# Performance work log

Hardware: AMD Instinct MI355X
Metric: run time of the kernel (lower is better)

## Reference

```python
import jax, jax.numpy as jnp
import numpy as np

DIM = 180
HEADS = 6
HID = 360
WINDOWS = ((8, 8), (16, 16))
SHIFTS0 = ((0, 0), (0, 0))
SHIFTS1 = ((4, 4), (8, 8))
EPS = 1e-5


def _bn(x, g, b, m, v):
    # eval-mode BatchNorm2d over [B,C,H,W]
    inv = g / jnp.sqrt(v + EPS)
    return x * inv[None, :, None, None] + (b - m * inv)[None, :, None, None]


def _conv1x1(x, w, b):
    return jnp.einsum('oc,bchw->bohw', w, x) + b[None, :, None, None]


def _shift_plus(x):
    # ShiftConv2d1x1 masked depthwise 3x3 == zero-padded single-pixel shifts per channel block
    c = x.shape[1] // 5
    pad = lambda a, spec: jnp.pad(a, ((0, 0), (0, 0)) + spec)
    g0 = pad(x[:, 0 * c:1 * c, :, 1:], ((0, 0), (0, 1)))   # out[y,x] = in[y,x+1]
    g1 = pad(x[:, 1 * c:2 * c, :, :-1], ((0, 0), (1, 0)))  # in[y,x-1]
    g2 = pad(x[:, 2 * c:3 * c, 1:, :], ((0, 1), (0, 0)))   # in[y+1,x]
    g3 = pad(x[:, 3 * c:4 * c, :-1, :], ((1, 0), (0, 0)))  # in[y-1,x]
    g4 = x[:, 4 * c:]
    return jnp.concatenate([g0, g1, g2, g3, g4], axis=1)


def _mlp(x, w1, b1, w2, b2):
    h = _conv1x1(_shift_plus(x), w1, b1)
    h = jax.nn.gelu(h, approximate=False)
    return _conv1x1(_shift_plus(h), w2, b2)


def _pixel_mixer(x):
    # circular-pad masked depthwise conv == circular rolls, channels interleaved mod 5
    B, C, H, W = x.shape
    xr = x.reshape(B, C // 5, 5, H, W)
    g0 = jnp.roll(xr[:, :, 0], -1, axis=-1)  # mask[m,2m]: in[y,(x+1)%W]
    g1 = jnp.roll(xr[:, :, 1], 1, axis=-1)   # mask[m,0]:  in[y,(x-1)%W]
    g2 = jnp.roll(xr[:, :, 2], -1, axis=-2)  # mask[2m,m]: in[(y+1)%H,x]
    g3 = jnp.roll(xr[:, :, 3], 1, axis=-2)   # mask[0,m]:  in[(y-1)%H,x]
    g4 = xr[:, :, 4]
    return jnp.stack([g0, g1, g2, g3, g4], axis=2).reshape(B, C, H, W)


def _swsa_slice(s, ws, shift):
    B, C, h, w = s.shape
    ph, pw = (-h) % ws[0], (-w) % ws[1]
    if ph or pw:
        s = jnp.pad(s, ((0, 0), (0, 0), (0, ph), (0, pw)), mode='reflect')
    if shift != (0, 0):
        s = jnp.roll(s, shift, axis=(2, 3))
    H, W = s.shape[2], s.shape[3]
    nh, nw = H // ws[0], W // ws[1]
    c = C // (2 * HEADS)
    # b (qv head c) (nh ws1) (nw ws2) -> qv b head nh nw (ws1 ws2) c
    s = s.reshape(B, 2, HEADS, c, nh, ws[0], nw, ws[1])
    s = s.transpose(1, 0, 2, 4, 6, 5, 7, 3).reshape(2, B, HEADS, nh, nw, ws[0] * ws[1], c)
    q, v = s[0], s[1]
    attn = jax.nn.softmax(jnp.einsum('...ic,...jc->...ij', q, q), axis=-1)
    o = jnp.einsum('...ij,...jc->...ic', attn, v)
    # -> b (head c) (nh ws1) (nw ws2)
    o = o.reshape(B, HEADS, nh, nw, ws[0], ws[1], c)
    o = o.transpose(0, 1, 6, 2, 4, 3, 5).reshape(B, HEADS * c, H, W)
    if shift != (0, 0):
        o = jnp.roll(o, (-shift[0], -shift[1]), axis=(2, 3))
    return o[:, :, :h, :w]


def _swsa(x, qkv_w, qkv_b, bn_g, bn_b, bn_m, bn_v, proj_w, proj_b, shifts):
    qkv = _bn(_conv1x1(x, qkv_w, qkv_b), bn_g, bn_b, bn_m, bn_v)
    C = qkv.shape[1]
    n = len(WINDOWS)
    outs = [_swsa_slice(qkv[:, i * (C // n):(i + 1) * (C // n)], ws, sh)
            for i, (ws, sh) in enumerate(zip(WINDOWS, shifts))]
    return _conv1x1(jnp.concatenate(outs, axis=1), proj_w, proj_b)


def _forward(x, a0_qkv_w, a0_qkv_b, a0_bn_g, a0_bn_b, a0_bn_m, a0_bn_v, a0_proj_w, a0_proj_b,
             a1_qkv_w, a1_qkv_b, a1_bn_g, a1_bn_b, a1_bn_m, a1_bn_v, a1_proj_w, a1_proj_b,
             t2_bn_g, t2_bn_b, t2_bn_m, t2_bn_v,
             m0_fc1_w, m0_fc1_b, m0_fc2_w, m0_fc2_b,
             m1_fc1_w, m1_fc1_b, m1_fc2_w, m1_fc2_b,
             m2_fc1_w, m2_fc1_b, m2_fc2_w, m2_fc2_b):
    # layer 0: SWSA (no shift) + Mlp
    x = x + _swsa(x, a0_qkv_w, a0_qkv_b, a0_bn_g, a0_bn_b, a0_bn_m, a0_bn_v, a0_proj_w, a0_proj_b, SHIFTS0)
    x = x + _mlp(x, m0_fc1_w, m0_fc1_b, m0_fc2_w, m0_fc2_b)
    # layer 1: SWSA (shifted) + Mlp
    x = x + _swsa(x, a1_qkv_w, a1_qkv_b, a1_bn_g, a1_bn_b, a1_bn_m, a1_bn_v, a1_proj_w, a1_proj_b, SHIFTS1)
    x = x + _mlp(x, m1_fc1_w, m1_fc1_b, m1_fc2_w, m1_fc2_b)
    # layer 2: TokenMixer + Mlp
    x = x + _bn(_pixel_mixer(x) - x, t2_bn_g, t2_bn_b, t2_bn_m, t2_bn_v)
    x = x + _mlp(x, m2_fc1_w, m2_fc1_b, m2_fc2_w, m2_fc2_b)
    return x


def setup_inputs() -> dict:
    keys = iter(jax.random.split(jax.random.key(0), 64))
    nrm = lambda s: jax.random.normal(next(keys), s, jnp.float32) * 0.02
    d, hd = DIM, HID
    inp = {'x': jax.random.normal(next(keys), (1, d, 256, 256), jnp.float32)}
    for i in range(2):
        inp[f'a{i}_qkv_w'] = nrm((2 * d, d))
        inp[f'a{i}_qkv_b'] = jnp.zeros((2 * d,), jnp.float32)
        inp[f'a{i}_bn_g'] = jnp.ones((2 * d,), jnp.float32)
        inp[f'a{i}_bn_b'] = jnp.zeros((2 * d,), jnp.float32)
        inp[f'a{i}_bn_m'] = jnp.zeros((2 * d,), jnp.float32)
        inp[f'a{i}_bn_v'] = jnp.ones((2 * d,), jnp.float32)
        inp[f'a{i}_proj_w'] = nrm((d, d))
        inp[f'a{i}_proj_b'] = jnp.zeros((d,), jnp.float32)
    inp['t2_bn_g'] = jnp.ones((d,), jnp.float32)
    inp['t2_bn_b'] = jnp.zeros((d,), jnp.float32)
    inp['t2_bn_m'] = jnp.zeros((d,), jnp.float32)
    inp['t2_bn_v'] = jnp.ones((d,), jnp.float32)
    for i in range(3):
        inp[f'm{i}_fc1_w'] = nrm((hd, d))
        inp[f'm{i}_fc1_b'] = jnp.zeros((hd,), jnp.float32)
        inp[f'm{i}_fc2_w'] = nrm((d, hd))
        inp[f'm{i}_fc2_b'] = jnp.zeros((d,), jnp.float32)
    return inp


def reference(x, a0_qkv_w, a0_qkv_b, a0_bn_g, a0_bn_b, a0_bn_m, a0_bn_v, a0_proj_w, a0_proj_b,
              a1_qkv_w, a1_qkv_b, a1_bn_g, a1_bn_b, a1_bn_m, a1_bn_v, a1_proj_w, a1_proj_b,
              t2_bn_g, t2_bn_b, t2_bn_m, t2_bn_v,
              m0_fc1_w, m0_fc1_b, m0_fc2_w, m0_fc2_b,
              m1_fc1_w, m1_fc1_b, m1_fc2_w, m1_fc2_b,
              m2_fc1_w, m2_fc1_b, m2_fc2_w, m2_fc2_b):
    return _forward(x, a0_qkv_w, a0_qkv_b, a0_bn_g, a0_bn_b, a0_bn_m, a0_bn_v, a0_proj_w, a0_proj_b,
                    a1_qkv_w, a1_qkv_b, a1_bn_g, a1_bn_b, a1_bn_m, a1_bn_v, a1_proj_w, a1_proj_b,
                    t2_bn_g, t2_bn_b, t2_bn_m, t2_bn_v,
                    m0_fc1_w, m0_fc1_b, m0_fc2_w, m0_fc2_b,
                    m1_fc1_w, m1_fc1_b, m1_fc2_w, m1_fc2_b,
                    m2_fc1_w, m2_fc1_b, m2_fc2_w, m2_fc2_b)
```

## Files before the change

kernel.cpp:

```cpp
#include <hip/hip_runtime.h>
#include <hip/hip_bf16.h>
#include <math.h>

#define P 65536

typedef float f32x4 __attribute__((ext_vector_type(4)));
typedef float f32x16 __attribute__((ext_vector_type(16)));
typedef short bf16x8 __attribute__((ext_vector_type(8)));
typedef unsigned short us8 __attribute__((ext_vector_type(8)));

__device__ __forceinline__ unsigned short f2b(float f) {
    __hip_bfloat16 h = __float2bfloat16(f);
    return __builtin_bit_cast(unsigned short, h);
}
__device__ __forceinline__ float b2f(unsigned short h) {
    return __builtin_bit_cast(float, (unsigned)h << 16);
}
__device__ __forceinline__ int shift_src(int g, int p) {
    int h = p >> 8, w = p & 255;
    if (g == 0) return (w < 255) ? p + 1 : -1;
    if (g == 1) return (w > 0) ? p - 1 : -1;
    if (g == 2) return (h < 255) ? p + 256 : -1;
    if (g == 3) return (h > 0) ? p - 256 : -1;
    return p;
}
__device__ __forceinline__ ushort4 cvt4(float4 f) {
    ushort4 o = {f2b(f.x), f2b(f.y), f2b(f.z), f2b(f.w)};
    return o;
}

__global__ __launch_bounds__(256) void to_nhwc(const float* __restrict__ x,
                                               unsigned short* __restrict__ Xb) {
    const int p = blockIdx.x * 256 + threadIdx.x;
    const int by = blockIdx.y;
    #pragma unroll
    for (int i = 0; i < 9; i++) {
        const int c4 = by * 9 + i;
        float4 v;
        v.x = x[(size_t)(c4 * 4 + 0) * P + p];
        v.y = x[(size_t)(c4 * 4 + 1) * P + p];
        v.z = x[(size_t)(c4 * 4 + 2) * P + p];
        v.w = x[(size_t)(c4 * 4 + 3) * P + p];
        *(ushort4*)&Xb[(size_t)p * 192 + c4 * 4] = cvt4(v);
    }
    if (by == 4) {
        ushort4 z4 = {0, 0, 0, 0};
        *(ushort4*)&Xb[(size_t)p * 192 + 180] = z4;
        *(ushort4*)&Xb[(size_t)p * 192 + 184] = z4;
        *(ushort4*)&Xb[(size_t)p * 192 + 188] = z4;
    }
}

struct WJobs {
    const float* W[10];
    const float* Bi[10];
    const float* G[10];
    const float* Bb[10];
    const float* M[10];
    const float* V[10];
    unsigned short* Wb[10];
    float* Sc[10];
    float* Sh[10];
    int OC[10];
    int K[10];
};
__global__ __launch_bounds__(256) void wcvtAll(WJobs j) {
    const int m = blockIdx.y;
    const int K = j.K[m];
    const int KP = (K == 180) ? 192 : 384;
    const int idx = blockIdx.x * 256 + threadIdx.x;
    if (idx >= 384 * KP) return;
    const int r = idx / KP, kp = idx - r * KP;
    const int rl = r % 192, rp = r / 192;
    const int kl = kp % 192, kpl = kp / 192;
    const int oc = (rl < 180) ? rp * 180 + rl : -1;
    const int k  = (kl < 180) ? kpl * 180 + kl : -1;
    const bool vld = (oc >= 0 && oc < j.OC[m]);
    unsigned short v = 0;
    if (vld && k >= 0 && k < K) v = f2b(j.W[m][(size_t)oc * K + k]);
    j.Wb[m][idx] = v;
    if (kp == 0) {
        float sc = 1.f, sh = 0.f;
        if (vld) {
            if (j.G[m]) {
                float inv = j.G[m][oc] * rsqrtf(j.V[m][oc] + 1e-5f);
                sc = inv;
                sh = j.Bb[m][oc] + (j.Bi[m][oc] - j.M[m][oc]) * inv;
            } else {
                sh = j.Bi[m][oc];
            }
        }
        j.Sc[m][r] = sc;
        j.Sh[m][r] = sh;
    }
}

template<int CIN, int SHIFT, int GELU, int RES, int CHW>
__global__ __launch_bounds__(512, 4) void mconv(
    const unsigned short* __restrict__ X0, const unsigned short* __restrict__ X1,
    const unsigned short* __restrict__ Wb,
    const float* __restrict__ Sc, const float* __restrict__ Sh,
    const unsigned short* __restrict__ Res,
    unsigned short* __restrict__ OutB0, unsigned short* __restrict__ OutB1,
    float* __restrict__ OutF)
{
    constexpr int KP = (CIN == 180) ? 192 : 384;
    constexpr int NCH = KP / 64;

    __shared__ __align__(16) unsigned short lx[128][76];
    __shared__ __align__(16) unsigned short lw[192][76];

    const int tid = threadIdx.x;
    const int lane = tid & 63, wid = tid >> 6;
    const int wp = wid >> 2, wo = wid & 3;
    const int pbase = blockIdx.x * 128;
    const int pl = blockIdx.y;
    Wb += (size_t)pl * 192 * KP;
    Sc += pl * 192;
    Sh += pl * 192;
    unsigned short* __restrict__ OutB = pl ? OutB1 : OutB0;

    f32x4 acc[3][4];
    #pragma unroll
    for (int a = 0; a < 3; a++)
        #pragma unroll
        for (int b = 0; b < 4; b++) acc[a][b] = (f32x4){0.f, 0.f, 0.f, 0.f};

    for (int ch = 0; ch < NCH; ++ch) {
        const int kc0 = ch * 64;
        if (ch) __syncthreads();
        #pragma unroll
        for (int i = 0; i < 3; i++) {
            int idx = tid + i * 512;
            int row = idx >> 3, c8 = (idx & 7) * 8;
            *(us8*)&lw[row][c8] = *(const us8*)&Wb[(size_t)row * KP + kc0 + c8];
        }
        if constexpr (CIN == 180 && !SHIFT) {
            #pragma unroll
            for (int i = 0; i < 2; i++) {
                int idx = tid + i * 512;
                int row = idx >> 3, c8 = (idx & 7) * 8;
                *(us8*)&lx[row][c8] = *(const us8*)&X0[(size_t)(pbase + row) * 192 + kc0 + c8];
            }
        } else if constexpr (CIN == 180) {
            #pragma unroll
            for (int i = 0; i < 4; i++) {
                int idx = tid + i * 512;
                int row = idx >> 4, c4 = kc0 + (idx & 15) * 4;
                int p = pbase + row;
                ushort4 hv = {0, 0, 0, 0};
                if (c4 < 180) {
                    int sp = shift_src(c4 / 36, p);
                    if (sp >= 0) hv = *(const ushort4*)&X0[(size_t)sp * 192 + c4];
                }
                *(ushort4*)&lx[row][c4 - kc0] = hv;
            }
        } else {
            const bool pl1 = (kc0 >= 192);
            const unsigned short* __restrict__ Xp = pl1 ? X1 : X0;
            const int kbase = kc0 - (pl1 ? 192 : 0);
            #pragma unroll
            for (int i = 0; i < 4; i++) {
                int idx = tid + i * 512;
                int row = idx >> 4, c4l = kbase + (idx & 15) * 4;
                int p = pbase + row;
                ushort4 hv = {0, 0, 0, 0};
                int k = (pl1 ? 180 : 0) + c4l;
                if (c4l < 180) {
                    if constexpr (SHIFT) {
                        int sp = shift_src(k / 72, p);
                        if (sp >= 0) hv = *(const ushort4*)&Xp[(size_t)sp * 192 + c4l];
                    } else {
                        hv = *(const ushort4*)&Xp[(size_t)p * 192 + c4l];
                    }
                }
                *(ushort4*)&lx[row][c4l - kbase] = hv;
            }
        }
        __syncthreads();
        #pragma unroll
        for (int ks = 0; ks < 2; ++ks) {
            const int ko = ks * 32 + (lane >> 4) * 8;
            bf16x8 av[3], bvv[4];
            #pragma unroll
            for (int m = 0; m < 3; m++)
                av[m] = *(const bf16x8*)&lw[wo * 48 + m * 16 + (lane & 15)][ko];
            #pragma unroll
            for (int n = 0; n < 4; n++)
                bvv[n] = *(const bf16x8*)&lx[wp * 64 + n * 16 + (lane & 15)][ko];
            #pragma unroll
            for (int m = 0; m < 3; m++)
                #pragma unroll
                for (int n = 0; n < 4; n++)
                    acc[m][n] = __builtin_amdgcn_mfma_f32_16x16x32_bf16(
                        av[m], bvv[n], acc[m][n], 0, 0, 0);
        }
    }

    #pragma unroll
    for (int m = 0; m < 3; ++m) {
        const int oc0 = wo * 48 + m * 16 + ((lane >> 4) * 4);
        if (oc0 >= 180) continue;
        float4 sc4 = *(const float4*)&Sc[oc0];
        float4 sh4 = *(const float4*)&Sh[oc0];
        #pragma unroll
        for (int n = 0; n < 4; ++n) {
            const int pix = pbase + wp * 64 + n * 16 + (lane & 15);
            float4 y;
            y.x = acc[m][n][0] * sc4.x + sh4.x;
            y.y = acc[m][n][1] * sc4.y + sh4.y;
            y.z = acc[m][n][2] * sc4.z + sh4.z;
            y.w = acc[m][n][3] * sc4.w + sh4.w;
            if constexpr (GELU) {
                y.x = 0.5f * y.x * (1.f + erff(y.x * 0.70710678118654752f));
                y.y = 0.5f * y.y * (1.f + erff(y.y * 0.70710678118654752f));
                y.z = 0.5f * y.z * (1.f + erff(y.z * 0.70710678118654752f));
                y.w = 0.5f * y.w * (1.f + erff(y.w * 0.70710678118654752f));
            }
            if constexpr (RES) {
                ushort4 rv = *(const ushort4*)&Res[(size_t)pix * 192 + oc0];
                y.x += b2f(rv.x);
                y.y += b2f(rv.y);
                y.z += b2f(rv.z);
                y.w += b2f(rv.w);
            }
            if constexpr (CHW) {
                OutF[(size_t)(oc0 + 0) * P + pix] = y.x;
                OutF[(size_t)(oc0 + 1) * P + pix] = y.y;
                OutF[(size_t)(oc0 + 2) * P + pix] = y.z;
                OutF[(size_t)(oc0 + 3) * P + pix] = y.w;
            } else {
                *(ushort4*)&OutB[(size_t)pix * 192 + oc0] = cvt4(y);
            }
        }
    }
}

template<int WSZ>
__device__ __forceinline__ void attn_body(const unsigned short* __restrict__ Qp,
                                          unsigned short* __restrict__ Ov, int sh,
                                          int bx, unsigned short* smem)
{
    constexpr int TOK = WSZ * WSZ;
    constexpr int WPB = (WSZ == 8) ? 4 : 1;
    constexpr int NMI = TOK / 32;

    unsigned short (*q_s)[24] = (unsigned short(*)[24])smem;
    unsigned short (*v_s)[16] = (unsigned short(*)[16])(smem + WPB * TOK * 24);

    const int tid = threadIdx.x;
    const int lane = tid & 63, wid = tid >> 6;
    const int la = lane & 31, h = lane >> 5;
    const int head = blockIdx.y;
    const int qoff = head * 15;
    const int obase = ((WSZ == 8) ? 0 : 90) + head * 15;

    const int win = (WSZ == 8) ? (bx * 4 + wid) : bx;
    const int wy = win >> ((WSZ == 8) ? 5 : 4);
    const int wx = win & ((WSZ == 8) ? 31 : 15);

    {
        const int sw = (WSZ == 8) ? wid : 0;
        const int t = (WSZ == 8) ? (tid & 63) : tid;
        const int ty = t / WSZ, tx = t % WSZ;
        const int gh = (wy * WSZ + ty - sh) & 255;
        const int gw = (wx * WSZ + tx - sh) & 255;
        const unsigned short* src = Qp + (size_t)((gh << 8) | gw) * 192 + qoff;
        #pragma unroll
        for (int c = 0; c < 15; c++) {
            q_s[sw * TOK + t][c] = src[c];
            v_s[sw * TOK + t][c] = src[90 + c];
        }
        q_s[sw * TOK + t][15] = 0;
        v_s[sw * TOK + t][15] = 0;
    }
    __syncthreads();

    const int mywin = (WSZ == 8) ? wid : 0;
    const unsigned short (*qs)[24] = &q_s[mywin * TOK];
    const unsigned short (*vs)[16] = &v_s[mywin * TOK];
    const int ni0 = (WSZ == 8) ? 0 : (wid * 2);
    const int ni1 = ni0 + 1;

    bf16x8 bfr0 = *(const bf16x8*)&qs[ni0 * 32 + la][h * 8];
    bf16x8 bfr1 = *(const bf16x8*)&qs[ni1 * 32 + la][h * 8];

    f32x16 O0, O1;
    #pragma unroll
    for (int r = 0; r < 16; r++) { O0[r] = 0.f; O1[r] = 0.f; }
    float m0 = -3.0e38f, m1 = -3.0e38f, l0 = 0.f, l1 = 0.f;

    unsigned short hw0[16], hw1[16];

    auto proc = [&](f32x16& S, float& m, float& l, f32x16& O, unsigned short* hw) {
        float vm = S[0];
        #pragma unroll
        for (int r = 1; r < 16; r++) vm = fmaxf(vm, S[r]);
        vm = fmaxf(vm, __shfl_xor(vm, 32));
        float nm = fmaxf(m, vm);
        float rs = __expf(m - nm);
        m = nm;
        l *= rs;
        #pragma unroll
        for (int r = 0; r < 16; r++) O[r] *= rs;
        float lacc = 0.f;
        #pragma unroll
        for (int r = 0; r < 16; r++) {
            unsigned short u = f2b(__expf(S[r] - nm));
            hw[r] = u;
            lacc += b2f(u);
        }
        l += lacc;
    };

    auto pack = [&](const unsigned short* hw, int sub) -> bf16x8 {
        unsigned A01 = (unsigned)hw[8 * sub + 0] | ((unsigned)hw[8 * sub + 1] << 16);
        unsigned A23 = (unsigned)hw[8 * sub + 2] | ((unsigned)hw[8 * sub + 3] << 16);
        unsigned B01 = (unsigned)hw[8 * sub + 4] | ((unsigned)hw[8 * sub + 5] << 16);
        unsigned B23 = (unsigned)hw[8 * sub + 6] | ((unsigned)hw[8 * sub + 7] << 16);
        unsigned x1 = (unsigned)__shfl_xor((int)(h ? A01 : B01), 32);
        unsigned x2 = (unsigned)__shfl_xor((int)(h ? A23 : B23), 32);
        union { unsigned u[4]; bf16x8 v; } pf;
        pf.u[0] = h ? x1 : A01;
        pf.u[1] = h ? x2 : A23;
        pf.u[2] = h ? B01 : x1;
        pf.u[3] = h ? B23 : x2;
        return pf.v;
    };

    for (int mi = 0; mi < NMI; ++mi) {
        bf16x8 af = *(const bf16x8*)&qs[mi * 32 + la][h * 8];
        f32x16 z;
        #pragma unroll
        for (int r = 0; r < 16; r++) z[r] = 0.f;
        f32x16 s0 = __builtin_amdgcn_mfma_f32_32x32x16_bf16(af, bfr0, z, 0, 0, 0);
        f32x16 s1 = __builtin_amdgcn_mfma_f32_32x32x16_bf16(af, bfr1, z, 0, 0, 0);

        proc(s0, m0, l0, O0, hw0);
        proc(s1, m1, l1, O1, hw1);

        #pragma unroll
        for (int sub = 0; sub < 2; ++sub) {
            union { unsigned short us[8]; bf16x8 v; } av;
            #pragma unroll
            for (int j = 0; j < 8; j++)
                av.us[j] = vs[mi * 32 + sub * 16 + h * 8 + j][la & 15];
            bf16x8 pf0 = pack(hw0, sub);
            bf16x8 pf1 = pack(hw1, sub);
            O0 = __builtin_amdgcn_mfma_f32_32x32x16_bf16(av.v, pf0, O0, 0, 0, 0);
            O1 = __builtin_amdgcn_mfma_f32_32x32x16_bf16(av.v, pf1, O1, 0, 0, 0);
        }
    }

    #pragma unroll
    for (int t = 0; t < 2; ++t) {
        const f32x16& O = t ? O1 : O0;
        float l = t ? l1 : l0;
        const int ni = t ? ni1 : ni0;
        float lt = l + __shfl_xor(l, 32);
        float inv = 1.f / lt;
        const int R = ni * 32 + la;
        const int ty = R / WSZ, tx = R % WSZ;
        const int gh = (wy * WSZ + ty - sh) & 255;
        const int gw = (wx * WSZ + tx - sh) & 255;
        unsigned short* dst = Ov + (size_t)((gh << 8) | gw) * 192 + obase;
        #pragma unroll
        for (int reg = 0; reg < 16; ++reg) {
            const int ch = (reg & 3) + 8 * (reg >> 2) + 4 * h;
            if (ch < 15) dst[ch] = f2b(O[reg] * inv);
        }
    }
}

__global__ __launch_bounds__(256) void mattn2(const unsigned short* __restrict__ Q0,
                                              const unsigned short* __restrict__ Q1,
                                              unsigned short* __restrict__ Av,
                                              int sh8, int sh16)
{
    __shared__ __align__(16) unsigned short smem[10240];
    if (blockIdx.x < 256) attn_body<8>(Q0, Av, sh8, blockIdx.x, smem);
    else                  attn_body<16>(Q1, Av, sh16, blockIdx.x - 256, smem);
}

__global__ __launch_bounds__(256) void pixmixk(const unsigned short* __restrict__ Xb,
    const float* __restrict__ g, const float* __restrict__ b,
    const float* __restrict__ m, const float* __restrict__ v,
    unsigned short* __restrict__ Yb)
{
    const int idx = blockIdx.x * 256 + threadIdx.x;
    const int p = idx / 45;
    const int c0 = (idx - p * 45) * 4;
    const int h = p >> 8, w = p & 255;
    ushort4 xv4 = *(const ushort4*)&Xb[(size_t)p * 192 + c0];
    ushort4 o;
    #pragma unroll
    for (int j = 0; j < 4; j++) {
        int c = c0 + j;
        int gr = c - (c / 5) * 5;
        int sp;
        if (gr == 0)      sp = (h << 8) | ((w + 1) & 255);
        else if (gr == 1) sp = (h << 8) | ((w - 1) & 255);
        else if (gr == 2) sp = (((h + 1) & 255) << 8) | w;
        else if (gr == 3) sp = (((h - 1) & 255) << 8) | w;
        else              sp = p;
        float pm = b2f(Xb[(size_t)sp * 192 + c]);
        float xv = b2f(((const unsigned short*)&xv4)[j]);
        float inv = g[c] * rsqrtf(v[c] + 1e-5f);
        float y = xv + (pm - xv - m[c]) * inv + b[c];
        ((unsigned short*)&o)[j] = f2b(y);
    }
    *(ushort4*)&Yb[(size_t)p * 192 + c0] = o;
}

extern "C" void kernel_launch(void* const* d_in, const int* in_sizes, int n_in,
                              void* d_out, int out_size, void* d_ws, size_t ws_size,
                              hipStream_t stream)
{
    const float* x        = (const float*)d_in[0];
    const float* a0_qkv_w = (const float*)d_in[1];
    const float* a0_qkv_b = (const float*)d_in[2];
    const float* a0_bn_g  = (const float*)d_in[3];
    const float* a0_bn_b  = (const float*)d_in[4];
    const float* a0_bn_m  = (const float*)d_in[5];
    const float* a0_bn_v  = (const float*)d_in[6];
    const float* a0_proj_w= (const float*)d_in[7];
    const float* a0_proj_b= (const float*)d_in[8];
    const float* a1_qkv_w = (const float*)d_in[9];
    const float* a1_qkv_b = (const float*)d_in[10];
    const float* a1_bn_g  = (const float*)d_in[11];
    const float* a1_bn_b  = (const float*)d_in[12];
    const float* a1_bn_m  = (const float*)d_in[13];
    const float* a1_bn_v  = (const float*)d_in[14];
    const float* a1_proj_w= (const float*)d_in[15];
    const float* a1_proj_b= (const float*)d_in[16];
    const float* t2_bn_g  = (const float*)d_in[17];
    const float* t2_bn_b  = (const float*)d_in[18];
    const float* t2_bn_m  = (const float*)d_in[19];
    const float* t2_bn_v  = (const float*)d_in[20];
    const float* m0_fc1_w = (const float*)d_in[21];
    const float* m0_fc1_b = (const float*)d_in[22];
    const float* m0_fc2_w = (const float*)d_in[23];
    const float* m0_fc2_b = (const float*)d_in[24];
    const float* m1_fc1_w = (const float*)d_in[25];
    const float* m1_fc1_b = (const float*)d_in[26];
    const float* m1_fc2_w = (const float*)d_in[27];
    const float* m1_fc2_b = (const float*)d_in[28];
    const float* m2_fc1_w = (const float*)d_in[29];
    const float* m2_fc1_b = (const float*)d_in[30];
    const float* m2_fc2_w = (const float*)d_in[31];
    const float* m2_fc2_b = (const float*)d_in[32];

    unsigned short* Q0  = (unsigned short*)d_ws;
    unsigned short* Q1  = Q0 + (size_t)P * 192;
    unsigned short* Ob  = Q1 + (size_t)P * 192;
    unsigned short* Av  = Ob + (size_t)P * 192;
    unsigned short* Wp  = Av + (size_t)P * 192;
    const size_t W192 = 384 * 192, W384 = (size_t)384 * 384;
    unsigned short* wb_qkv0 = Wp;
    unsigned short* wb_prj0 = wb_qkv0 + W192;
    unsigned short* wb_qkv1 = wb_prj0 + W192;
    unsigned short* wb_prj1 = wb_qkv1 + W192;
    unsigned short* wb_fc1_0 = wb_prj1 + W192;
    unsigned short* wb_fc1_1 = wb_fc1_0 + W192;
    unsigned short* wb_fc1_2 = wb_fc1_1 + W192;
    unsigned short* wb_fc2_0 = wb_fc1_2 + W192;
    unsigned short* wb_fc2_1 = wb_fc2_0 + W384;
    unsigned short* wb_fc2_2 = wb_fc2_1 + W384;
    float* ScA = (float*)(wb_fc2_2 + W384);
    float* ShA = ScA + 10 * 384;

    dim3 blk(256);
    dim3 blk512(512);
    dim3 gA(512, 2);
    dim3 gB(512);
    dim3 gAt(512, 6);

    WJobs jobs;
    for (int i = 0; i < 10; i++) { jobs.G[i] = nullptr; jobs.Bb[i] = nullptr; jobs.M[i] = nullptr; jobs.V[i] = nullptr; }
    jobs.W[0] = a0_qkv_w;  jobs.Bi[0] = a0_qkv_b;  jobs.Wb[0] = wb_qkv0;  jobs.OC[0] = 360; jobs.K[0] = 180;
    jobs.G[0] = a0_bn_g; jobs.Bb[0] = a0_bn_b; jobs.M[0] = a0_bn_m; jobs.V[0] = a0_bn_v;
    jobs.W[1] = a0_proj_w; jobs.Bi[1] = a0_proj_b; jobs.Wb[1] = wb_prj0;  jobs.OC[1] = 180; jobs.K[1] = 180;
    jobs.W[2] = a1_qkv_w;  jobs.Bi[2] = a1_qkv_b;  jobs.Wb[2] = wb_qkv1;  jobs.OC[2] = 360; jobs.K[2] = 180;
    jobs.G[2] = a1_bn_g; jobs.Bb[2] = a1_bn_b; jobs.M[2] = a1_bn_m; jobs.V[2] = a1_bn_v;
    jobs.W[3] = a1_proj_w; jobs.Bi[3] = a1_proj_b; jobs.Wb[3] = wb_prj1;  jobs.OC[3] = 180; jobs.K[3] = 180;
    jobs.W[4] = m0_fc1_w;  jobs.Bi[4] = m0_fc1_b;  jobs.Wb[4] = wb_fc1_0; jobs.OC[4] = 360; jobs.K[4] = 180;
    jobs.W[5] = m1_fc1_w;  jobs.Bi[5] = m1_fc1_b;  jobs.Wb[5] = wb_fc1_1; jobs.OC[5] = 360; jobs.K[5] = 180;
    jobs.W[6] = m2_fc1_w;  jobs.Bi[6] = m2_fc1_b;  jobs.Wb[6] = wb_fc1_2; jobs.OC[6] = 360; jobs.K[6] = 180;
    jobs.W[7] = m0_fc2_w;  jobs.Bi[7] = m0_fc2_b;  jobs.Wb[7] = wb_fc2_0; jobs.OC[7] = 180; jobs.K[7] = 360;
    jobs.W[8] = m1_fc2_w;  jobs.Bi[8] = m1_fc2_b;  jobs.Wb[8] = wb_fc2_1; jobs.OC[8] = 180; jobs.K[8] = 360;
    jobs.W[9] = m2_fc2_w;  jobs.Bi[9] = m2_fc2_b;  jobs.Wb[9] = wb_fc2_2; jobs.OC[9] = 180; jobs.K[9] = 360;
    for (int i = 0; i < 10; i++) { jobs.Sc[i] = ScA + i * 384; jobs.Sh[i] = ShA + i * 384; }
    wcvtAll<<<dim3(576, 10), blk, 0, stream>>>(jobs);
    to_nhwc<<<dim3(256, 5), blk, 0, stream>>>(x, Ob);

    mconv<180,0,0,0,0><<<gA, blk512, 0, stream>>>(Ob, nullptr, wb_qkv0,
        ScA + 0 * 384, ShA + 0 * 384, nullptr, Q0, Q1, nullptr);
    mattn2<<<gAt, blk, 0, stream>>>(Q0, Q1, Av, 0, 0);
    mconv<180,0,0,1,0><<<gB, blk512, 0, stream>>>(Av, nullptr, wb_prj0,
        ScA + 1 * 384, ShA + 1 * 384, Ob, Ob, nullptr, nullptr);

    mconv<180,1,1,0,0><<<gA, blk512, 0, stream>>>(Ob, nullptr, wb_fc1_0,
        ScA + 4 * 384, ShA + 4 * 384, nullptr, Q0, Q1, nullptr);
    mconv<360,1,0,1,0><<<gB, blk512, 0, stream>>>(Q0, Q1, wb_fc2_0,
        ScA + 7 * 384, ShA + 7 * 384, Ob, Ob, nullptr, nullptr);

    mconv<180,0,0,0,0><<<gA, blk512, 0, stream>>>(Ob, nullptr, wb_qkv1,
        ScA + 2 * 384, ShA + 2 * 384, nullptr, Q0, Q1, nullptr);
    mattn2<<<gAt, blk, 0, stream>>>(Q0, Q1, Av, 4, 8);
    mconv<180,0,0,1,0><<<gB, blk512, 0, stream>>>(Av, nullptr, wb_prj1,
        ScA + 3 * 384, ShA + 3 * 384, Ob, Ob, nullptr, nullptr);

    mconv<180,1,1,0,0><<<gA, blk512, 0, stream>>>(Ob, nullptr, wb_fc1_1,
        ScA + 5 * 384, ShA + 5 * 384, nullptr, Q0, Q1, nullptr);
    mconv<360,1,0,1,0><<<gB, blk512, 0, stream>>>(Q0, Q1, wb_fc2_1,
        ScA + 8 * 384, ShA + 8 * 384, Ob, Ob, nullptr, nullptr);

    pixmixk<<<dim3(65536 * 45 / 256), blk, 0, stream>>>(Ob, t2_bn_g, t2_bn_b,
        t2_bn_m, t2_bn_v, Av);

    mconv<180,1,1,0,0><<<gA, blk512, 0, stream>>>(Av, nullptr, wb_fc1_2,
        ScA + 6 * 384, ShA + 6 * 384, nullptr, Q0, Q1, nullptr);
    mconv<360,1,0,1,1><<<gB, blk512, 0, stream>>>(Q0, Q1, wb_fc2_2,
        ScA + 9 * 384, ShA + 9 * 384, Av, nullptr, nullptr, (float*)d_out);
}
```

Measured before the change: 503.0 us.

## Pad QKV output layout to 16-channel head slots for vectorized attention loads

```diff
diff --git a/kernel.cpp b/kernel.cpp
--- a/kernel.cpp
+++ b/kernel.cpp
@@ -63,6 +63,7 @@
     float* Sh[10];
     int OC[10];
     int K[10];
+    int QKV[10];
 };
 __global__ __launch_bounds__(256) void wcvtAll(WJobs j) {
     const int m = blockIdx.y;
@@ -73,7 +74,13 @@
     const int r = idx / KP, kp = idx - r * KP;
     const int rl = r % 192, rp = r / 192;
     const int kl = kp % 192, kpl = kp / 192;
-    const int oc = (rl < 180) ? rp * 180 + rl : -1;
+    int oc;
+    if (j.QKV[m]) {
+        const int half = rl / 96, hh = (rl % 96) / 16, ii = rl % 16;
+        oc = (ii < 15) ? rp * 180 + half * 90 + hh * 15 + ii : -1;
+    } else {
+        oc = (rl < 180) ? rp * 180 + rl : -1;
+    }
     const int k  = (kl < 180) ? kpl * 180 + kl : -1;
     const bool vld = (oc >= 0 && oc < j.OC[m]);
     unsigned short v = 0;
@@ -95,7 +102,7 @@
     }
 }
 
-template<int CIN, int SHIFT, int GELU, int RES, int CHW>
+template<int CIN, int SHIFT, int GELU, int RES, int CHW, int QKVL = 0>
 __global__ __launch_bounds__(512, 4) void mconv(
     const unsigned short* __restrict__ X0, const unsigned short* __restrict__ X1,
     const unsigned short* __restrict__ Wb,
@@ -200,7 +207,7 @@
     #pragma unroll
     for (int m = 0; m < 3; ++m) {
         const int oc0 = wo * 48 + m * 16 + ((lane >> 4) * 4);
-        if (oc0 >= 180) continue;
+        if constexpr (!QKVL) { if (oc0 >= 180) continue; }
         float4 sc4 = *(const float4*)&Sc[oc0];
         float4 sh4 = *(const float4*)&Sh[oc0];
         #pragma unroll
@@ -237,9 +244,9 @@
 }
 
 template<int WSZ>
-__device__ __forceinline__ void attn_body(const unsigned short* __restrict__ Qp,
-                                          unsigned short* __restrict__ Ov, int sh,
-                                          int bx, unsigned short* smem)
+__device__ void attn_body(const unsigned short* __restrict__ Qp,
+                          unsigned short* __restrict__ Ov, int sh,
+                          int bx, int head, unsigned short* smem)
 {
     constexpr int TOK = WSZ * WSZ;
     constexpr int WPB = (WSZ == 8) ? 4 : 1;
@@ -251,8 +258,6 @@
     const int tid = threadIdx.x;
     const int lane = tid & 63, wid = tid >> 6;
     const int la = lane & 31, h = lane >> 5;
-    const int head = blockIdx.y;
-    const int qoff = head * 15;
     const int obase = ((WSZ == 8) ? 0 : 90) + head * 15;
 
     const int win = (WSZ == 8) ? (bx * 4 + wid) : bx;
@@ -265,14 +270,15 @@
         const int ty = t / WSZ, tx = t % WSZ;
         const int gh = (wy * WSZ + ty - sh) & 255;
         const int gw = (wx * WSZ + tx - sh) & 255;
-        const unsigned short* src = Qp + (size_t)((gh << 8) | gw) * 192 + qoff;
-        #pragma unroll
-        for (int c = 0; c < 15; c++) {
-            q_s[sw * TOK + t][c] = src[c];
-            v_s[sw * TOK + t][c] = src[90 + c];
-        }
-        q_s[sw * TOK + t][15] = 0;
-        v_s[sw * TOK + t][15] = 0;
+        const unsigned short* src = Qp + (size_t)((gh << 8) | gw) * 192 + head * 16;
+        us8 q0 = *(const us8*)&src[0];
+        us8 q1 = *(const us8*)&src[8];
+        us8 v0 = *(const us8*)&src[96];
+        us8 v1 = *(const us8*)&src[104];
+        *(us8*)&q_s[sw * TOK + t][0] = q0;
+        *(us8*)&q_s[sw * TOK + t][8] = q1;
+        *(us8*)&v_s[sw * TOK + t][0] = v0;
+        *(us8*)&v_s[sw * TOK + t][8] = v1;
     }
     __syncthreads();
 
@@ -378,8 +384,9 @@
                                               int sh8, int sh16)
 {
     __shared__ __align__(16) unsigned short smem[10240];
-    if (blockIdx.x < 256) attn_body<8>(Q0, Av, sh8, blockIdx.x, smem);
-    else                  attn_body<16>(Q1, Av, sh16, blockIdx.x - 256, smem);
+    const int head = blockIdx.y;
+    if (blockIdx.x < 256) attn_body<8>(Q0, Av, sh8, blockIdx.x, head, smem);
+    else                  attn_body<16>(Q1, Av, sh16, blockIdx.x - 256, head, smem);
 }
 
 __global__ __launch_bounds__(256) void pixmixk(const unsigned short* __restrict__ Xb,
@@ -476,12 +483,12 @@
     dim3 gAt(512, 6);
 
     WJobs jobs;
-    for (int i = 0; i < 10; i++) { jobs.G[i] = nullptr; jobs.Bb[i] = nullptr; jobs.M[i] = nullptr; jobs.V[i] = nullptr; }
+    for (int i = 0; i < 10; i++) { jobs.G[i] = nullptr; jobs.Bb[i] = nullptr; jobs.M[i] = nullptr; jobs.V[i] = nullptr; jobs.QKV[i] = 0; }
     jobs.W[0] = a0_qkv_w;  jobs.Bi[0] = a0_qkv_b;  jobs.Wb[0] = wb_qkv0;  jobs.OC[0] = 360; jobs.K[0] = 180;
-    jobs.G[0] = a0_bn_g; jobs.Bb[0] = a0_bn_b; jobs.M[0] = a0_bn_m; jobs.V[0] = a0_bn_v;
+    jobs.G[0] = a0_bn_g; jobs.Bb[0] = a0_bn_b; jobs.M[0] = a0_bn_m; jobs.V[0] = a0_bn_v; jobs.QKV[0] = 1;
     jobs.W[1] = a0_proj_w; jobs.Bi[1] = a0_proj_b; jobs.Wb[1] = wb_prj0;  jobs.OC[1] = 180; jobs.K[1] = 180;
     jobs.W[2] = a1_qkv_w;  jobs.Bi[2] = a1_qkv_b;  jobs.Wb[2] = wb_qkv1;  jobs.OC[2] = 360; jobs.K[2] = 180;
-    jobs.G[2] = a1_bn_g; jobs.Bb[2] = a1_bn_b; jobs.M[2] = a1_bn_m; jobs.V[2] = a1_bn_v;
+    jobs.G[2] = a1_bn_g; jobs.Bb[2] = a1_bn_b; jobs.M[2] = a1_bn_m; jobs.V[2] = a1_bn_v; jobs.QKV[2] = 1;
     jobs.W[3] = a1_proj_w; jobs.Bi[3] = a1_proj_b; jobs.Wb[3] = wb_prj1;  jobs.OC[3] = 180; jobs.K[3] = 180;
     jobs.W[4] = m0_fc1_w;  jobs.Bi[4] = m0_fc1_b;  jobs.Wb[4] = wb_fc1_0; jobs.OC[4] = 360; jobs.K[4] = 180;
     jobs.W[5] = m1_fc1_w;  jobs.Bi[5] = m1_fc1_b;  jobs.Wb[5] = wb_fc1_1; jobs.OC[5] = 360; jobs.K[5] = 180;
@@ -493,7 +500,7 @@
     wcvtAll<<<dim3(576, 10), blk, 0, stream>>>(jobs);
     to_nhwc<<<dim3(256, 5), blk, 0, stream>>>(x, Ob);
 
-    mconv<180,0,0,0,0><<<gA, blk512, 0, stream>>>(Ob, nullptr, wb_qkv0,
+    mconv<180,0,0,0,0,1><<<gA, blk512, 0, stream>>>(Ob, nullptr, wb_qkv0,
         ScA + 0 * 384, ShA + 0 * 384, nullptr, Q0, Q1, nullptr);
     mattn2<<<gAt, blk, 0, stream>>>(Q0, Q1, Av, 0, 0);
     mconv<180,0,0,1,0><<<gB, blk512, 0, stream>>>(Av, nullptr, wb_prj0,
@@ -504,7 +511,7 @@
     mconv<360,1,0,1,0><<<gB, blk512, 0, stream>>>(Q0, Q1, wb_fc2_0,
         ScA + 7 * 384, ShA + 7 * 384, Ob, Ob, nullptr, nullptr);
 
-    mconv<180,0,0,0,0><<<gA, blk512, 0, stream>>>(Ob, nullptr, wb_qkv1,
+    mconv<180,0,0,0,0,1><<<gA, blk512, 0, stream>>>(Ob, nullptr, wb_qkv1,
         ScA + 2 * 384, ShA + 2 * 384, nullptr, Q0, Q1, nullptr);
     mattn2<<<gAt, blk, 0, stream>>>(Q0, Q1, Av, 4, 8);
     mconv<180,0,0,1,0><<<gB, blk512, 0, stream>>>(Av, nullptr, wb_prj1,
```

Result: faster. 484.8 us (-3.6%).
